# Optimization experiments

Hardware: AMD Instinct MI355X
Metric: run time of the kernel (lower is better)

Reference implementation:

```python
import jax, jax.numpy as jnp
import numpy as np
import math

B, S, D = 2, 2048, 2048
H = 16
HD = D // H          # 128
LAT = 512            # latent_dim


def setup_inputs() -> dict:
    key = jax.random.key(0)
    ks = jax.random.split(key, 8)
    x = jax.random.normal(ks[0], (B, S, D), dtype=jnp.float32)
    freqs = jax.random.uniform(ks[1], (S, HD // 2), dtype=jnp.float32) * (2 * math.pi)
    # additive causal mask: 0 on/below diagonal, -1e9 above
    causal = jnp.tril(jnp.ones((S, S), dtype=bool))
    mask = jnp.where(causal, 0.0, -1e9).astype(jnp.float32)
    sc = 0.02
    Wq = jax.random.normal(ks[2], (D, H * HD), dtype=jnp.float32) * sc
    Wdown = jax.random.normal(ks[3], (D, LAT), dtype=jnp.float32) * sc
    Wkup = jax.random.normal(ks[4], (LAT, H * HD), dtype=jnp.float32) * sc
    Wvup = jax.random.normal(ks[5], (LAT, H * HD), dtype=jnp.float32) * sc
    Wo = jax.random.normal(ks[6], (D, D), dtype=jnp.float32) * sc
    return {"x": x, "freqs": freqs, "mask": mask,
            "Wq": Wq, "Wdown": Wdown, "Wkup": Wkup, "Wvup": Wvup, "Wo": Wo}


def _apply_rope(t, cos, sin):
    # t: [B, S, H, HD]; cos/sin: [1, S, 1, HD//2]
    tp = t.reshape(t.shape[:-1] + (HD // 2, 2))
    t0, t1 = tp[..., 0], tp[..., 1]
    rot = jnp.stack([t0 * cos - t1 * sin, t0 * sin + t1 * cos], axis=-1)
    return rot.reshape(t.shape)


def reference(x, freqs, mask, Wq, Wdown, Wkup, Wvup, Wo):
    b, s, d = x.shape
    Q = (x @ Wq).reshape(b, s, H, HD)
    c_kv = x @ Wdown                       # [B, S, LAT] low-rank latent
    K = (c_kv @ Wkup).reshape(b, s, H, HD)
    V = (c_kv @ Wvup).reshape(b, s, H, HD)
    cos = jnp.cos(freqs)[None, :, None, :]
    sin = jnp.sin(freqs)[None, :, None, :]
    Q = _apply_rope(Q, cos, sin)
    K = _apply_rope(K, cos, sin)
    scores = jnp.einsum('bqhd,bkhd->bhqk', Q, K) / math.sqrt(HD)
    scores = scores + mask                 # [S,S] broadcast over [B,H,S,S]
    probs = jax.nn.softmax(scores, axis=-1)
    attn = jnp.einsum('bhqk,bkhd->bqhd', probs, V).reshape(b, s, d)
    return attn @ Wo
```

## Files before the change

### kernel.cpp

```cpp
#include <hip/hip_runtime.h>
#include <hip/hip_bf16.h>
#include <math.h>

typedef __hip_bfloat16 bf16;
typedef __attribute__((ext_vector_type(8))) short short8;
typedef __attribute__((ext_vector_type(4))) float f32x4;

static constexpr int BB   = 2;
static constexpr int SS   = 2048;
static constexpr int DD   = 2048;
static constexpr int NH   = 16;
static constexpr int HDD  = 128;
static constexpr int LATD = 512;
static constexpr int MR   = BB * SS;
static constexpr int QRS  = DD + LATD;

#if __has_builtin(__builtin_amdgcn_exp2f)
#define EXP2F(x) __builtin_amdgcn_exp2f(x)
#else
#define EXP2F(x) exp2f(x)
#endif

__device__ __forceinline__ void async_cp16(const void* g, void* l) {
    __builtin_amdgcn_global_load_lds(
        (const __attribute__((address_space(1))) void*)g,
        (__attribute__((address_space(3))) void*)l, 16, 0, 0);
}

__device__ __forceinline__ unsigned short bf_bits(bf16 v) {
    union { bf16 b; unsigned short u; } cv; cv.b = v; return cv.u;
}

template <int CTRL>
__device__ __forceinline__ float dpp_mov(float x) {
    int r = __builtin_amdgcn_update_dpp(0, __float_as_int(x), CTRL, 0xF, 0xF, true);
    return __int_as_float(r);
}
__device__ __forceinline__ float dpp_max16(float x) {
    x = fmaxf(x, dpp_mov<0xB1>(x));
    x = fmaxf(x, dpp_mov<0x4E>(x));
    x = fmaxf(x, dpp_mov<0x141>(x));
    x = fmaxf(x, dpp_mov<0x140>(x));
    return x;
}
__device__ __forceinline__ float dpp_sum16(float x) {
    x += dpp_mov<0xB1>(x);
    x += dpp_mov<0x4E>(x);
    x += dpp_mov<0x141>(x);
    x += dpp_mov<0x140>(x);
    return x;
}

__global__ __launch_bounds__(256) void prep(
    const float* __restrict__ x, bf16* __restrict__ xb,
    const float* __restrict__ Wq, const float* __restrict__ Wdown,
    const float* __restrict__ Wkup, const float* __restrict__ Wvup,
    bf16* __restrict__ WqdT, bf16* __restrict__ WkvT) {
    __shared__ float tile[32][33];
    const int blk = blockIdx.x, tid = threadIdx.x;
    if (blk < 8192) {
        const int i = blk * 256 + tid;
        float4 v = ((const float4*)x)[i];
        ushort4 o;
        o.x = bf_bits(__float2bfloat16(v.x));
        o.y = bf_bits(__float2bfloat16(v.y));
        o.z = bf_bits(__float2bfloat16(v.z));
        o.w = bf_bits(__float2bfloat16(v.w));
        ((ushort4*)xb)[i] = o;
        return;
    }
    const float* in; bf16* out; int rows, cols, bx, by;
    if (blk < 12288) {
        const int l = blk - 8192;  in = Wq;    out = WqdT;
        rows = DD;   cols = DD;    bx = l & 63; by = l >> 6;
    } else if (blk < 13312) {
        const int l = blk - 12288; in = Wdown; out = WqdT + (size_t)DD * DD;
        rows = DD;   cols = LATD;  bx = l & 15; by = l >> 4;
    } else if (blk < 14336) {
        const int l = blk - 13312; in = Wkup;  out = WkvT;
        rows = LATD; cols = DD;    bx = l & 63; by = l >> 6;
    } else {
        const int l = blk - 14336; in = Wvup;  out = WkvT + (size_t)DD * LATD;
        rows = LATD; cols = DD;    bx = l & 63; by = l >> 6;
    }
    const int tx = tid & 31, ty = tid >> 5;
    const int c0 = bx * 32, r0 = by * 32;
    for (int i = 0; i < 32; i += 8)
        tile[ty + i][tx] = in[(size_t)(r0 + ty + i) * cols + c0 + tx];
    __syncthreads();
    for (int i = 0; i < 32; i += 8)
        out[(size_t)(c0 + ty + i) * rows + r0 + tx] =
            __float2bfloat16(tile[tx][ty + i]);
}

template <bool OUT_F32>
__global__ __launch_bounds__(256) void gemm_bt(
    const bf16* __restrict__ A, const bf16* __restrict__ Bt,
    void* __restrict__ Cout, int M, int N, int K, int lda, int ldb, int ldc) {
    __shared__ bf16 As[2][128 * 32];
    __shared__ bf16 Bs[2][128 * 32];
    const int tid  = threadIdx.x;
    const int lane = tid & 63, wave = tid >> 6;
    const int quad = lane >> 4, l16 = lane & 15;
    const int row0 = blockIdx.y * 128, col0 = blockIdx.x * 128;
    const int wm = (wave >> 1) * 64, wn = (wave & 1) * 64;
    const int srow = lane >> 2;
    const int scol = (lane & 3) * 8;

    f32x4 acc[4][4];
    for (int i = 0; i < 4; ++i)
        for (int j = 0; j < 4; ++j)
            for (int r = 0; r < 4; ++r) acc[i][j][r] = 0.f;

    auto stage = [&](int k0, int bufi) {
        for (int c = 0; c < 2; ++c) {
            const int chunk = wave * 2 + c;
            const int r = chunk * 16 + srow;
            async_cp16(A  + (size_t)(row0 + r) * lda + k0 + scol, &As[bufi][chunk * 512]);
            async_cp16(Bt + (size_t)(col0 + r) * ldb + k0 + scol, &Bs[bufi][chunk * 512]);
        }
    };

    const int nk = K / 32;
    stage(0, 0);
    for (int ki = 0; ki < nk; ++ki) {
        __syncthreads();
        if (ki + 1 < nk) stage((ki + 1) * 32, (ki + 1) & 1);
        const int bi = ki & 1;
        short8 af[4], bfr[4];
        for (int t = 0; t < 4; ++t) {
            af[t]  = *(const short8*)&As[bi][(wm + t * 16 + l16) * 32 + quad * 8];
            bfr[t] = *(const short8*)&Bs[bi][(wn + t * 16 + l16) * 32 + quad * 8];
        }
        for (int i = 0; i < 4; ++i)
            for (int j = 0; j < 4; ++j)
                acc[i][j] = __builtin_amdgcn_mfma_f32_16x16x32_bf16(
                    af[i], bfr[j], acc[i][j], 0, 0, 0);
    }

    const int rbase = row0 + wm + quad * 4;
    const int cbase = col0 + wn + l16;
    if (OUT_F32) {
        float* C = (float*)Cout;
        for (int i = 0; i < 4; ++i)
            for (int j = 0; j < 4; ++j)
                for (int r = 0; r < 4; ++r)
                    C[(size_t)(rbase + i * 16 + r) * ldc + cbase + j * 16] = acc[i][j][r];
    } else {
        bf16* C = (bf16*)Cout;
        for (int i = 0; i < 4; ++i)
            for (int j = 0; j < 4; ++j)
                for (int r = 0; r < 4; ++r)
                    C[(size_t)(rbase + i * 16 + r) * ldc + cbase + j * 16] =
                        __float2bfloat16(acc[i][j][r]);
    }
}

__global__ __launch_bounds__(256) void tvrope(
    bf16* __restrict__ KV, bf16* __restrict__ VT,
    const float* __restrict__ freqs,
    const float* __restrict__ Wo, bf16* __restrict__ WoT) {
    __shared__ __align__(16) char sm[64 * 74 * 2];
    const int blk = blockIdx.x, tid = threadIdx.x;
    if (blk < 2048) {
        bf16 (*t)[74] = (bf16(*)[74])sm;
        const int bx = blk & 31, byy = (blk >> 5) & 1, bh = blk >> 6;
        const int s0 = bx * 64, d0 = byy * 64;
        const int b = bh >> 4, h = bh & 15;
        const bf16* src = KV + (size_t)b * SS * 4096 + 2048 + h * 128 + d0;
        for (int p = 0; p < 2; ++p) {
            const int s = p * 32 + (tid >> 3), dc = (tid & 7) * 8;
            short8 v = *(const short8*)(src + (size_t)(s0 + s) * 4096 + dc);
            const bf16* ve = (const bf16*)&v;
            for (int e = 0; e < 8; ++e) t[s][dc + e] = ve[e];
        }
        __syncthreads();
        bf16* dst = VT + ((size_t)bh * HDD + d0) * SS + s0;
        for (int p = 0; p < 2; ++p) {
            const int d = p * 32 + (tid >> 3), g = tid & 7;
            short8 v; bf16* ve = (bf16*)&v;
            for (int e = 0; e < 8; ++e) ve[e] = t[g * 8 + e][d];
            const int gp = g ^ (d & 7);
            *(short8*)(dst + (size_t)d * SS + gp * 8) = v;
        }
        return;
    }
    if (blk < 6144) {
        const int idx = (blk - 2048) * 256 + tid;
        const int pg  = idx & 15;
        const int h   = (idx >> 4) & (NH - 1);
        const int tok = idx >> 8;
        const int s   = tok & (SS - 1);
        const float4 f = *(const float4*)&freqs[s * 64 + pg * 4];
        const float fr[4] = {f.x, f.y, f.z, f.w};
        bf16* kp = KV + (size_t)tok * 4096 + h * HDD + pg * 8;
        short8 v = *(const short8*)kp;
        const bf16* ve = (const bf16*)&v;
        short8 o; bf16* oe = (bf16*)&o;
        for (int i = 0; i < 4; ++i) {
            const float cs = __cosf(fr[i]), sn = __sinf(fr[i]);
            const float t0 = __bfloat162float(ve[2 * i]);
            const float t1 = __bfloat162float(ve[2 * i + 1]);
            oe[2 * i]     = __float2bfloat16(t0 * cs - t1 * sn);
            oe[2 * i + 1] = __float2bfloat16(t0 * sn + t1 * cs);
        }
        *(short8*)kp = o;
        return;
    }
    {
        float (*tile)[33] = (float(*)[33])sm;
        const int l = blk - 6144;
        const int bx = l & 63, by = l >> 6;
        const int tx = tid & 31, ty = tid >> 5;
        const int c0 = bx * 32, r0 = by * 32;
        for (int i = 0; i < 32; i += 8)
            tile[ty + i][tx] = Wo[(size_t)(r0 + ty + i) * DD + c0 + tx];
        __syncthreads();
        for (int i = 0; i < 32; i += 8)
            WoT[(size_t)(c0 + ty + i) * DD + r0 + tx] =
                __float2bfloat16(tile[tx][ty + i]);
    }
}

__global__ __launch_bounds__(512, 4) void flash_attn(
    const bf16* __restrict__ QC, const bf16* __restrict__ KV,
    const bf16* __restrict__ VTg, const float* __restrict__ freqs,
    bf16* __restrict__ O) {
    const int j = blockIdx.x;
    const int bh = (j >> 3) & 31, q3 = j & 7;
    const int qt = (j & 256) ? q3 : 15 - q3;
    const int h = bh & (NH - 1), b = bh >> 4;
    const int q0 = qt * 128;
    const int tid = threadIdx.x, lane = tid & 63, wave = tid >> 6;
    const int quad = lane >> 4, l16 = lane & 15;

    __shared__ char smem[81920];
    bf16* KsB = (bf16*)smem;
    bf16* VtB = (bf16*)(smem + 32768);
    bf16* PsB = (bf16*)(smem + 65536);

    const bf16* Kb  = KV  + (size_t)b * SS * 4096 + h * HDD;
    const bf16* VTb = VTg + (size_t)bh * HDD * SS;
    const int krs = 4096;

    const float QS = 0.08838834764831845f * 1.4426950408889634f;
    short8 qf[4];
    {
        const int s = q0 + wave * 16 + l16;
        const bf16* qrow = QC + (size_t)(b * SS + s) * QRS + h * HDD;
        for (int kk = 0; kk < 4; ++kk) {
            short8 v = *(const short8*)(qrow + kk * 32 + quad * 8);
            const float4 f = *(const float4*)&freqs[s * 64 + kk * 16 + quad * 4];
            const float fr[4] = {f.x, f.y, f.z, f.w};
            const bf16* ve = (const bf16*)&v;
            bf16* oe = (bf16*)&qf[kk];
            for (int i = 0; i < 4; ++i) {
                const float cs = __cosf(fr[i]), sn = __sinf(fr[i]);
                const float t0 = __bfloat162float(ve[2 * i]);
                const float t1 = __bfloat162float(ve[2 * i + 1]);
                oe[2 * i]     = __float2bfloat16((t0 * cs - t1 * sn) * QS);
                oe[2 * i + 1] = __float2bfloat16((t0 * sn + t1 * cs) * QS);
            }
        }
    }

    const int kk_s = wave >> 1, half_s = wave & 1;
    const bf16* Ksrc = Kb + ((size_t)(half_s * 32) + (lane >> 2)) * krs
                          + kk_s * 32 + (lane & 3) * 8;
    const bf16* Vsrc = VTb + ((size_t)(wave * 16) + (lane >> 3)) * SS + (lane & 7) * 8;

    auto stage = [&](int kt, int bufi) {
        const size_t koffK = (size_t)kt * 64 * krs;
        const int k0 = kt * 64;
        for (int i = 0; i < 2; ++i)
            async_cp16(Ksrc + koffK + (size_t)i * 16 * krs,
                       &KsB[bufi * 8192 + kk_s * 2048 + (half_s * 32 + i * 16) * 32]);
        for (int c2 = 0; c2 < 2; ++c2)
            async_cp16(Vsrc + (size_t)c2 * 8 * SS + k0,
                       &VtB[bufi * 8192 + (wave * 2 + c2) * 512]);
    };

    f32x4 accO[8];
    for (int i = 0; i < 8; ++i)
        for (int r = 0; r < 4; ++r) accO[i][r] = 0.f;
    float m_r[4], l_r[4];
    for (int r = 0; r < 4; ++r) { m_r[r] = -1e30f; l_r[r] = 0.f; }

    const int ktMax = 2 * qt + 1;
    const int qwTop = q0 + wave * 16 + 15;

    stage(0, 0);
    for (int kt = 0; kt <= ktMax; ++kt) {
        const int k0 = kt * 64;
        __syncthreads();
        if (kt < ktMax) stage(kt + 1, (kt + 1) & 1);
        const int bi = kt & 1;

        if (k0 > qwTop) continue;

        f32x4 sfr[4];
        for (int nt = 0; nt < 4; ++nt)
            for (int r = 0; r < 4; ++r) sfr[nt][r] = 0.f;
        __builtin_amdgcn_s_setprio(1);
        for (int kk = 0; kk < 4; ++kk)
            for (int nt = 0; nt < 4; ++nt) {
                short8 kf = *(const short8*)
                    &KsB[bi * 8192 + kk * 2048 + (nt * 16 + l16) * 32 + quad * 8];
                sfr[nt] = __builtin_amdgcn_mfma_f32_16x16x32_bf16(
                    qf[kk], kf, sfr[nt], 0, 0, 0);
            }
        __builtin_amdgcn_s_setprio(0);

        float sv[4][4];
        for (int nt = 0; nt < 4; ++nt)
            for (int r = 0; r < 4; ++r) sv[nt][r] = sfr[nt][r];
        if (kt >= 2 * qt) {
            const int qg = q0 + wave * 16 + quad * 4;
            for (int nt = 0; nt < 4; ++nt) {
                const int kgl = k0 + nt * 16 + l16;
                for (int r = 0; r < 4; ++r)
                    if (kgl > qg + r) sv[nt][r] = -1e30f;
            }
        }
        float rmax[4];
        for (int r = 0; r < 4; ++r) {
            float m = fmaxf(fmaxf(sv[0][r], sv[1][r]), fmaxf(sv[2][r], sv[3][r]));
            rmax[r] = dpp_max16(m);
        }
        const bool grow = (rmax[0] > m_r[0] + 8.f) || (rmax[1] > m_r[1] + 8.f) ||
                          (rmax[2] > m_r[2] + 8.f) || (rmax[3] > m_r[3] + 8.f);
        if (__any(grow)) {
            float alpha[4];
            for (int r = 0; r < 4; ++r) {
                const float mnew = fmaxf(m_r[r], rmax[r]);
                alpha[r] = EXP2F(m_r[r] - mnew);
                m_r[r] = mnew;
                l_r[r] *= alpha[r];
            }
            for (int nt = 0; nt < 8; ++nt)
                for (int r = 0; r < 4; ++r) accO[nt][r] *= alpha[r];
        }
        float psum[4] = {0.f, 0.f, 0.f, 0.f};
        for (int nt = 0; nt < 4; ++nt)
            for (int r = 0; r < 4; ++r) {
                const float p = EXP2F(sv[nt][r] - m_r[r]);
                sv[nt][r] = p;
                psum[r] += p;
            }
        for (int r = 0; r < 4; ++r) l_r[r] += dpp_sum16(psum[r]);

        for (int nt = 0; nt < 4; ++nt)
            for (int r = 0; r < 4; ++r) {
                const int row = quad * 4 + r;
                const int g = nt * 2 + (l16 >> 3);
                PsB[wave * 1024 + row * 64 + ((g ^ (row & 7)) << 3) + (l16 & 7)] =
                    __float2bfloat16(sv[nt][r]);
            }
        __builtin_amdgcn_s_waitcnt(0xc07f);

        __builtin_amdgcn_s_setprio(1);
        for (int ks = 0; ks < 2; ++ks) {
            const int gp = ((ks * 4 + quad) ^ (l16 & 7)) << 3;
            short8 pf = *(const short8*)&PsB[wave * 1024 + l16 * 64 + gp];
            for (int nt = 0; nt < 8; ++nt) {
                const int d = nt * 16 + l16;
                short8 vf = *(const short8*)&VtB[bi * 8192 + d * 64 + gp];
                accO[nt] = __builtin_amdgcn_mfma_f32_16x16x32_bf16(
                    pf, vf, accO[nt], 0, 0, 0);
            }
        }
        __builtin_amdgcn_s_setprio(0);
        __builtin_amdgcn_s_waitcnt(0xc07f);
    }

    bf16* Ob = O + (size_t)b * SS * DD + h * HDD;
    float inv[4];
    for (int r = 0; r < 4; ++r) inv[r] = 1.f / l_r[r];
    for (int nt = 0; nt < 8; ++nt)
        for (int r = 0; r < 4; ++r)
            Ob[(size_t)(q0 + wave * 16 + quad * 4 + r) * DD + nt * 16 + l16] =
                __float2bfloat16(accO[nt][r] * inv[r]);
}

extern "C" void kernel_launch(void* const* d_in, const int* in_sizes, int n_in,
                              void* d_out, int out_size, void* d_ws, size_t ws_size,
                              hipStream_t stream) {
    (void)in_sizes; (void)n_in; (void)out_size; (void)ws_size;
    const float* x     = (const float*)d_in[0];
    const float* freqs = (const float*)d_in[1];
    const float* Wq    = (const float*)d_in[3];
    const float* Wdown = (const float*)d_in[4];
    const float* Wkup  = (const float*)d_in[5];
    const float* Wvup  = (const float*)d_in[6];
    const float* Wo    = (const float*)d_in[7];
    float* out = (float*)d_out;

    char* ws = (char*)d_ws;
    size_t off = 0;
    auto take = [&](size_t bytes) -> void* {
        void* p = ws + off;
        off += (bytes + 255) & ~(size_t)255;
        return p;
    };
    bf16* xb    = (bf16*)take((size_t)MR * DD * 2);
    bf16* WqdT  = (bf16*)take((size_t)QRS * DD * 2);
    bf16* WkvT  = (bf16*)take((size_t)2 * DD * LATD * 2);
    bf16* QC    = (bf16*)take((size_t)MR * QRS * 2);
    bf16* KVb   = (bf16*)take((size_t)MR * 2 * DD * 2);
    bf16* VTg   = (bf16*)take((size_t)BB * NH * HDD * SS * 2);
    bf16* attn  = xb;
    bf16* WoT   = WqdT;

    prep<<<15360, 256, 0, stream>>>(x, xb, Wq, Wdown, Wkup, Wvup, WqdT, WkvT);

    gemm_bt<false><<<dim3(QRS / 128, MR / 128), 256, 0, stream>>>(
        xb, WqdT, QC, MR, QRS, DD, DD, DD, QRS);
    gemm_bt<false><<<dim3(2 * DD / 128, MR / 128), 256, 0, stream>>>(
        QC + DD, WkvT, KVb, MR, 2 * DD, LATD, QRS, LATD, 2 * DD);

    tvrope<<<10240, 256, 0, stream>>>(KVb, VTg, freqs, Wo, WoT);

    flash_attn<<<512, 512, 0, stream>>>(QC, KVb, VTg, freqs, attn);

    gemm_bt<true><<<dim3(DD / 128, MR / 128), 256, 0, stream>>>(
        attn, WoT, out, MR, DD, DD, DD, DD, DD);
}
```

Measured before the change: 347.2 us.

## Rewrite flash attention with 32x32x16 MFMA, S-transposed tiles and register P

The flash attention kernel moves from 16x16x32 to 32x32x16 bf16 MFMA, with 4 waves each owning 32 query rows instead of 8 waves owning 16. Scores are computed as K·Q^T, so each lane holds one query row, which makes the row max and sum mostly lane-local. P is then passed to the PV MFMA through cross-half shuffles instead of an LDS round trip, and the K tile gets an XOR-swizzled layout. The intent is fewer LDS transfers and less reduction overhead per tile. In exchange the kernel carries more registers per thread and has half the waves per block, which can reduce latency hiding.

```diff
diff --git a/kernel.cpp b/kernel.cpp
--- a/kernel.cpp
+++ b/kernel.cpp
@@ -5,6 +5,7 @@
 typedef __hip_bfloat16 bf16;
 typedef __attribute__((ext_vector_type(8))) short short8;
 typedef __attribute__((ext_vector_type(4))) float f32x4;
+typedef __attribute__((ext_vector_type(16))) float f32x16;
 
 static constexpr int BB   = 2;
 static constexpr int SS   = 2048;
@@ -29,26 +30,6 @@
 
 __device__ __forceinline__ unsigned short bf_bits(bf16 v) {
     union { bf16 b; unsigned short u; } cv; cv.b = v; return cv.u;
-}
-
-template <int CTRL>
-__device__ __forceinline__ float dpp_mov(float x) {
-    int r = __builtin_amdgcn_update_dpp(0, __float_as_int(x), CTRL, 0xF, 0xF, true);
-    return __int_as_float(r);
-}
-__device__ __forceinline__ float dpp_max16(float x) {
-    x = fmaxf(x, dpp_mov<0xB1>(x));
-    x = fmaxf(x, dpp_mov<0x4E>(x));
-    x = fmaxf(x, dpp_mov<0x141>(x));
-    x = fmaxf(x, dpp_mov<0x140>(x));
-    return x;
-}
-__device__ __forceinline__ float dpp_sum16(float x) {
-    x += dpp_mov<0xB1>(x);
-    x += dpp_mov<0x4E>(x);
-    x += dpp_mov<0x141>(x);
-    x += dpp_mov<0x140>(x);
-    return x;
 }
 
 __global__ __launch_bounds__(256) void prep(
@@ -222,7 +203,7 @@
     }
 }
 
-__global__ __launch_bounds__(512, 4) void flash_attn(
+__global__ __launch_bounds__(256, 2) void flash_attn(
     const bf16* __restrict__ QC, const bf16* __restrict__ KV,
     const bf16* __restrict__ VTg, const float* __restrict__ freqs,
     bf16* __restrict__ O) {
@@ -232,62 +213,63 @@
     const int h = bh & (NH - 1), b = bh >> 4;
     const int q0 = qt * 128;
     const int tid = threadIdx.x, lane = tid & 63, wave = tid >> 6;
-    const int quad = lane >> 4, l16 = lane & 15;
-
-    __shared__ char smem[81920];
-    bf16* KsB = (bf16*)smem;
-    bf16* VtB = (bf16*)(smem + 32768);
-    bf16* PsB = (bf16*)(smem + 65536);
+    const int l32 = lane & 31, hi = lane >> 5;
+
+    __shared__ __align__(16) char smem[66048];
+    bf16*  KsB  = (bf16*)smem;
+    bf16*  VtB  = (bf16*)(smem + 32768);
+    float* RedS = (float*)(smem + 65536);
 
     const bf16* Kb  = KV  + (size_t)b * SS * 4096 + h * HDD;
     const bf16* VTb = VTg + (size_t)bh * HDD * SS;
-    const int krs = 4096;
 
     const float QS = 0.08838834764831845f * 1.4426950408889634f;
-    short8 qf[4];
+    const int qrow = q0 + wave * 32 + l32;
+    short8 qf[8];
     {
-        const int s = q0 + wave * 16 + l16;
-        const bf16* qrow = QC + (size_t)(b * SS + s) * QRS + h * HDD;
-        for (int kk = 0; kk < 4; ++kk) {
-            short8 v = *(const short8*)(qrow + kk * 32 + quad * 8);
-            const float4 f = *(const float4*)&freqs[s * 64 + kk * 16 + quad * 4];
+        const bf16* qp = QC + (size_t)(b * SS + qrow) * QRS + h * HDD;
+#pragma unroll
+        for (int dk = 0; dk < 8; ++dk) {
+            short8 v = *(const short8*)(qp + dk * 16 + hi * 8);
+            const float4 f = *(const float4*)&freqs[(size_t)qrow * 64 + dk * 8 + hi * 4];
             const float fr[4] = {f.x, f.y, f.z, f.w};
             const bf16* ve = (const bf16*)&v;
-            bf16* oe = (bf16*)&qf[kk];
-            for (int i = 0; i < 4; ++i) {
-                const float cs = __cosf(fr[i]), sn = __sinf(fr[i]);
-                const float t0 = __bfloat162float(ve[2 * i]);
-                const float t1 = __bfloat162float(ve[2 * i + 1]);
-                oe[2 * i]     = __float2bfloat16((t0 * cs - t1 * sn) * QS);
-                oe[2 * i + 1] = __float2bfloat16((t0 * sn + t1 * cs) * QS);
+            bf16* oe = (bf16*)&qf[dk];
+#pragma unroll
+            for (int i2 = 0; i2 < 4; ++i2) {
+                const float cs = __cosf(fr[i2]), sn = __sinf(fr[i2]);
+                const float t0 = __bfloat162float(ve[2 * i2]);
+                const float t1 = __bfloat162float(ve[2 * i2 + 1]);
+                oe[2 * i2]     = __float2bfloat16((t0 * cs - t1 * sn) * QS);
+                oe[2 * i2 + 1] = __float2bfloat16((t0 * sn + t1 * cs) * QS);
             }
         }
     }
 
-    const int kk_s = wave >> 1, half_s = wave & 1;
-    const bf16* Ksrc = Kb + ((size_t)(half_s * 32) + (lane >> 2)) * krs
-                          + kk_s * 32 + (lane & 3) * 8;
-    const bf16* Vsrc = VTb + ((size_t)(wave * 16) + (lane >> 3)) * SS + (lane & 7) * 8;
-
     auto stage = [&](int kt, int bufi) {
-        const size_t koffK = (size_t)kt * 64 * krs;
         const int k0 = kt * 64;
-        for (int i = 0; i < 2; ++i)
-            async_cp16(Ksrc + koffK + (size_t)i * 16 * krs,
-                       &KsB[bufi * 8192 + kk_s * 2048 + (half_s * 32 + i * 16) * 32]);
-        for (int c2 = 0; c2 < 2; ++c2)
-            async_cp16(Vsrc + (size_t)c2 * 8 * SS + k0,
-                       &VtB[bufi * 8192 + (wave * 2 + c2) * 512]);
+#pragma unroll
+        for (int ii = 0; ii < 4; ++ii) {
+            const int i = wave * 4 + ii;
+            const int krow = 4 * i + (lane >> 4);
+            const int csrc = (lane & 15) ^ (krow & 7);
+            async_cp16(Kb + (size_t)(k0 + krow) * 4096 + csrc * 8,
+                       KsB + bufi * 8192 + i * 512);
+            const int d = 8 * i + (lane >> 3);
+            async_cp16(VTb + (size_t)d * SS + k0 + (lane & 7) * 8,
+                       VtB + bufi * 8192 + i * 512);
+        }
     };
 
-    f32x4 accO[8];
-    for (int i = 0; i < 8; ++i)
-        for (int r = 0; r < 4; ++r) accO[i][r] = 0.f;
-    float m_r[4], l_r[4];
-    for (int r = 0; r < 4; ++r) { m_r[r] = -1e30f; l_r[r] = 0.f; }
+    f32x16 accO[4];
+#pragma unroll
+    for (int d = 0; d < 4; ++d)
+#pragma unroll
+        for (int r = 0; r < 16; ++r) accO[d][r] = 0.f;
+    float m_r = -1e30f, l_r = 0.f;
 
     const int ktMax = 2 * qt + 1;
-    const int qwTop = q0 + wave * 16 + 15;
+    const int qwb = q0 + wave * 32;
 
     stage(0, 0);
     for (int kt = 0; kt <= ktMax; ++kt) {
@@ -296,90 +278,126 @@
         if (kt < ktMax) stage(kt + 1, (kt + 1) & 1);
         const int bi = kt & 1;
 
-        if (k0 > qwTop) continue;
-
-        f32x4 sfr[4];
-        for (int nt = 0; nt < 4; ++nt)
-            for (int r = 0; r < 4; ++r) sfr[nt][r] = 0.f;
+        if (k0 > qwb + 31) continue;
+
+        f32x16 st[2];
+#pragma unroll
+        for (int t = 0; t < 2; ++t)
+#pragma unroll
+            for (int r = 0; r < 16; ++r) st[t][r] = 0.f;
         __builtin_amdgcn_s_setprio(1);
-        for (int kk = 0; kk < 4; ++kk)
-            for (int nt = 0; nt < 4; ++nt) {
+#pragma unroll
+        for (int dk = 0; dk < 8; ++dk)
+#pragma unroll
+            for (int t = 0; t < 2; ++t) {
+                const int rd = t * 32 + l32;
                 short8 kf = *(const short8*)
-                    &KsB[bi * 8192 + kk * 2048 + (nt * 16 + l16) * 32 + quad * 8];
-                sfr[nt] = __builtin_amdgcn_mfma_f32_16x16x32_bf16(
-                    qf[kk], kf, sfr[nt], 0, 0, 0);
+                    &KsB[bi * 8192 + rd * 128 + ((((dk << 1) | hi) ^ (rd & 7)) << 3)];
+                st[t] = __builtin_amdgcn_mfma_f32_32x32x16_bf16(
+                    kf, qf[dk], st[t], 0, 0, 0);
             }
         __builtin_amdgcn_s_setprio(0);
 
-        float sv[4][4];
-        for (int nt = 0; nt < 4; ++nt)
-            for (int r = 0; r < 4; ++r) sv[nt][r] = sfr[nt][r];
-        if (kt >= 2 * qt) {
-            const int qg = q0 + wave * 16 + quad * 4;
-            for (int nt = 0; nt < 4; ++nt) {
-                const int kgl = k0 + nt * 16 + l16;
-                for (int r = 0; r < 4; ++r)
-                    if (kgl > qg + r) sv[nt][r] = -1e30f;
+        float p[32];
+#pragma unroll
+        for (int t = 0; t < 2; ++t)
+#pragma unroll
+            for (int r = 0; r < 16; ++r) p[t * 16 + r] = st[t][r];
+
+        if (k0 + 63 > qwb) {
+#pragma unroll
+            for (int t = 0; t < 2; ++t)
+#pragma unroll
+                for (int r = 0; r < 16; ++r) {
+                    const int kv = k0 + t * 32 + (r & 3) + 8 * (r >> 2) + 4 * hi;
+                    if (kv > qrow) p[t * 16 + r] = -1e30f;
+                }
+        }
+
+        float mt[16];
+#pragma unroll
+        for (int n = 0; n < 16; ++n) mt[n] = fmaxf(p[n], p[n + 16]);
+#pragma unroll
+        for (int n = 0; n < 8; ++n) mt[n] = fmaxf(mt[n], mt[n + 8]);
+#pragma unroll
+        for (int n = 0; n < 4; ++n) mt[n] = fmaxf(mt[n], mt[n + 4]);
+        float mx = fmaxf(fmaxf(mt[0], mt[1]), fmaxf(mt[2], mt[3]));
+        const float rmax = fmaxf(mx, __shfl_xor(mx, 32));
+
+        const bool grow = rmax > m_r + 8.f;
+        if (__any(grow)) {
+            const float mnew = fmaxf(m_r, rmax);
+            const float alpha = EXP2F(m_r - mnew);
+            m_r = mnew;
+            l_r *= alpha;
+            RedS[wave * 32 + l32] = alpha;
+            __builtin_amdgcn_s_waitcnt(0xc07f);
+#pragma unroll
+            for (int r = 0; r < 16; ++r) {
+                const float av = RedS[wave * 32 + ((r & 3) + 8 * (r >> 2) + 4 * hi)];
+#pragma unroll
+                for (int d = 0; d < 4; ++d) accO[d][r] *= av;
             }
         }
-        float rmax[4];
-        for (int r = 0; r < 4; ++r) {
-            float m = fmaxf(fmaxf(sv[0][r], sv[1][r]), fmaxf(sv[2][r], sv[3][r]));
-            rmax[r] = dpp_max16(m);
-        }
-        const bool grow = (rmax[0] > m_r[0] + 8.f) || (rmax[1] > m_r[1] + 8.f) ||
-                          (rmax[2] > m_r[2] + 8.f) || (rmax[3] > m_r[3] + 8.f);
-        if (__any(grow)) {
-            float alpha[4];
-            for (int r = 0; r < 4; ++r) {
-                const float mnew = fmaxf(m_r[r], rmax[r]);
-                alpha[r] = EXP2F(m_r[r] - mnew);
-                m_r[r] = mnew;
-                l_r[r] *= alpha[r];
+
+#pragma unroll
+        for (int r = 0; r < 32; ++r) p[r] = EXP2F(p[r] - m_r);
+        float sa[16];
+#pragma unroll
+        for (int n = 0; n < 16; ++n) sa[n] = p[n] + p[n + 16];
+#pragma unroll
+        for (int n = 0; n < 8; ++n) sa[n] += sa[n + 8];
+#pragma unroll
+        for (int n = 0; n < 4; ++n) sa[n] += sa[n + 4];
+        float ps = (sa[0] + sa[1]) + (sa[2] + sa[3]);
+        l_r += ps + __shfl_xor(ps, 32);
+
+        unsigned int pk[16];
+#pragma unroll
+        for (int n = 0; n < 16; ++n) {
+            const unsigned int lo = bf_bits(__float2bfloat16(p[2 * n]));
+            const unsigned int hl = bf_bits(__float2bfloat16(p[2 * n + 1]));
+            pk[n] = lo | (hl << 16);
+        }
+
+#pragma unroll
+        for (int m = 0; m < 4; ++m) {
+            const int A0 = 4 * m;
+            const unsigned int op0 = __shfl_xor(pk[A0 + 0], 32);
+            const unsigned int op1 = __shfl_xor(pk[A0 + 1], 32);
+            const unsigned int op2 = __shfl_xor(pk[A0 + 2], 32);
+            const unsigned int op3 = __shfl_xor(pk[A0 + 3], 32);
+            union { unsigned int w[4]; short8 s; } fr;
+            fr.w[0] = hi ? op2 : pk[A0 + 0];
+            fr.w[1] = hi ? op3 : pk[A0 + 1];
+            fr.w[2] = hi ? pk[A0 + 2] : op0;
+            fr.w[3] = hi ? pk[A0 + 3] : op1;
+            __builtin_amdgcn_s_setprio(1);
+#pragma unroll
+            for (int db = 0; db < 4; ++db) {
+                const int d = db * 32 + l32;
+                short8 vf = *(const short8*)
+                    &VtB[bi * 8192 + d * 64 + ((((m << 1) | hi) ^ (d & 7)) << 3)];
+                accO[db] = __builtin_amdgcn_mfma_f32_32x32x16_bf16(
+                    fr.s, vf, accO[db], 0, 0, 0);
             }
-            for (int nt = 0; nt < 8; ++nt)
-                for (int r = 0; r < 4; ++r) accO[nt][r] *= alpha[r];
-        }
-        float psum[4] = {0.f, 0.f, 0.f, 0.f};
-        for (int nt = 0; nt < 4; ++nt)
-            for (int r = 0; r < 4; ++r) {
-                const float p = EXP2F(sv[nt][r] - m_r[r]);
-                sv[nt][r] = p;
-                psum[r] += p;
-            }
-        for (int r = 0; r < 4; ++r) l_r[r] += dpp_sum16(psum[r]);
-
-        for (int nt = 0; nt < 4; ++nt)
-            for (int r = 0; r < 4; ++r) {
-                const int row = quad * 4 + r;
-                const int g = nt * 2 + (l16 >> 3);
-                PsB[wave * 1024 + row * 64 + ((g ^ (row & 7)) << 3) + (l16 & 7)] =
-                    __float2bfloat16(sv[nt][r]);
-            }
-        __builtin_amdgcn_s_waitcnt(0xc07f);
-
-        __builtin_amdgcn_s_setprio(1);
-        for (int ks = 0; ks < 2; ++ks) {
-            const int gp = ((ks * 4 + quad) ^ (l16 & 7)) << 3;
-            short8 pf = *(const short8*)&PsB[wave * 1024 + l16 * 64 + gp];
-            for (int nt = 0; nt < 8; ++nt) {
-                const int d = nt * 16 + l16;
-                short8 vf = *(const short8*)&VtB[bi * 8192 + d * 64 + gp];
-                accO[nt] = __builtin_amdgcn_mfma_f32_16x16x32_bf16(
-                    pf, vf, accO[nt], 0, 0, 0);
-            }
-        }
-        __builtin_amdgcn_s_setprio(0);
-        __builtin_amdgcn_s_waitcnt(0xc07f);
-    }
-
+            __builtin_amdgcn_s_setprio(0);
+        }
+    }
+
+    const float invl = 1.f / l_r;
+    RedS[wave * 32 + l32] = invl;
+    __builtin_amdgcn_s_waitcnt(0xc07f);
     bf16* Ob = O + (size_t)b * SS * DD + h * HDD;
-    float inv[4];
-    for (int r = 0; r < 4; ++r) inv[r] = 1.f / l_r[r];
-    for (int nt = 0; nt < 8; ++nt)
-        for (int r = 0; r < 4; ++r)
-            Ob[(size_t)(q0 + wave * 16 + quad * 4 + r) * DD + nt * 16 + l16] =
-                __float2bfloat16(accO[nt][r] * inv[r]);
+#pragma unroll
+    for (int r = 0; r < 16; ++r) {
+        const int row = (r & 3) + 8 * (r >> 2) + 4 * hi;
+        const float iv = RedS[wave * 32 + row];
+        const size_t ro = (size_t)(q0 + wave * 32 + row) * DD;
+#pragma unroll
+        for (int db = 0; db < 4; ++db)
+            Ob[ro + db * 32 + l32] = __float2bfloat16(accO[db][r] * iv);
+    }
 }
 
 extern "C" void kernel_launch(void* const* d_in, const int* in_sizes, int n_in,
@@ -420,7 +438,7 @@
 
     tvrope<<<10240, 256, 0, stream>>>(KVb, VTg, freqs, Wo, WoT);
 
-    flash_attn<<<512, 512, 0, stream>>>(QC, KVb, VTg, freqs, attn);
+    flash_attn<<<512, 256, 0, stream>>>(QC, KVb, VTg, freqs, attn);
 
     gemm_bt<true><<<dim3(DD / 128, MR / 128), 256, 0, stream>>>(
         attn, WoT, out, MR, DD, DD, DD, DD, DD);
```

New measurement: 347.3 us. No clear change (+0.0%).
